# Performance work log

Hardware: AMD Instinct MI355X
Metric: run time of the kernel (lower is better)

## Reference

```python
import jax, jax.numpy as jnp
import numpy as np
from jax import lax

B, C, H, W = 32, 256, 56, 56
OUT_C, K, M = 256, 3, 8
STRIDE = (1, 1)
PADDING = ((1, 1), (1, 1))


def setup_inputs() -> dict:
    key = jax.random.key(0)
    ks = jax.random.split(key, 5)
    x = jax.random.normal(ks[0], (B, C, H, W), dtype=jnp.float32)
    # expert kernels: (M, out_C, in_C/groups, kh, kw), init like torch.randn*0.02
    weight = jax.random.normal(ks[1], (M, OUT_C, C, K, K), dtype=jnp.float32) * 0.02
    bias = jnp.zeros((M, OUT_C), dtype=jnp.float32)
    # gate Linear(in=C, out=M): torch stores weight as (out, in)
    bound = 1.0 / np.sqrt(C)
    gate_w = jax.random.uniform(ks[2], (M, C), minval=-bound, maxval=bound, dtype=jnp.float32)
    gate_b = jax.random.uniform(ks[3], (M,), minval=-bound, maxval=bound, dtype=jnp.float32)
    return {"x": x, "weight": weight, "bias": bias, "gate_w": gate_w, "gate_b": gate_b}


def reference(x, weight, bias, gate_w, gate_b):
    # global average pool -> gating
    gap = jnp.mean(x, axis=(2, 3))                         # (B, C)
    alpha = jax.nn.softmax(gap @ gate_w.T + gate_b, axis=1)  # (B, M)
    # per-sample combined kernels and biases
    kernels = jnp.einsum('bm,moikl->boikl', alpha, weight)  # (B, O, I, k, k)
    biases = alpha @ bias                                   # (B, O)

    def conv_one(xi, wi):
        # xi: (C,H,W), wi: (O,I,k,k)
        out = lax.conv_general_dilated(
            xi[None], wi,
            window_strides=STRIDE, padding=PADDING,
            dimension_numbers=('NCHW', 'OIHW', 'NCHW'))
        return out[0]  # (O, H, W)

    out = jax.vmap(conv_one)(x, kernels)                    # (B, O, H, W)
    return out + biases[:, :, None, None]
```

## Files before the change

kernel.cpp:

```cpp
#include <hip/hip_runtime.h>
#include <hip/hip_bf16.h>

#define B_    32
#define C_    256
#define HW_   3136
#define OC_   256
#define M_    8
#define KPB_  589824

typedef short v8s __attribute__((ext_vector_type(8)));
typedef float f32x4 __attribute__((ext_vector_type(4)));

union bf8pack { v8s v; __hip_bfloat16 h[8]; };

__device__ __forceinline__ void gll16(const short* src, short* dst) {
    __builtin_amdgcn_global_load_lds((const __attribute__((address_space(1))) void*)src,
                                     (__attribute__((address_space(3))) void*)dst, 16, 0, 0);
}

__global__ void zero_gap_kernel(float* __restrict__ gap) {
    gap[blockIdx.x * 256 + threadIdx.x] = 0.f;
}

__global__ __launch_bounds__(256) void xcast_kernel(const float* __restrict__ x,
                                                    short* __restrict__ xg,
                                                    float* __restrict__ gap) {
    __shared__ __hip_bfloat16 tile[64][65];
    int b = blockIdx.z, ct = blockIdx.y, pt = blockIdx.x;
    int p0 = pt*64, c0 = ct*64;
    int tp = threadIdx.x & 63, tc = threadIdx.x >> 6;
    const float* xb = x + ((size_t)b*C_ + c0) * HW_ + p0;
    #pragma unroll
    for (int j = 0; j < 16; ++j) {
        int cl = tc + j*4;
        float v = xb[(size_t)cl*HW_ + tp];
        tile[cl][tp] = __float2bfloat16(v);
        float s = v;
        #pragma unroll
        for (int off = 32; off; off >>= 1) s += __shfl_xor(s, off, 64);
        if (tp == 0) atomicAdd(&gap[b*C_ + c0 + cl], s);
    }
    __syncthreads();
    #pragma unroll
    for (int it = 0; it < 2; ++it) {
        int idx = it*256 + threadIdx.x;
        int px = idx >> 3, ck = idx & 7;
        bf8pack pk;
        #pragma unroll
        for (int j = 0; j < 8; ++j) pk.h[j] = tile[ck*8 + j][px];
        int c = c0 + ck*8;
        size_t dst = (((size_t)b*8 + (c >> 5))*HW_ + p0 + px)*32 + (c & 31);
        *(v8s*)(xg + dst) = pk.v;
    }
}

__global__ void alpha_kernel(const float* __restrict__ gap,
                             const float* __restrict__ gate_w,
                             const float* __restrict__ gate_b,
                             const float* __restrict__ bias,
                             float* __restrict__ alpha,
                             float* __restrict__ biasc) {
    int b = blockIdx.x, lane = threadIdx.x;
    const float inv = 1.0f / HW_;
    float g0 = gap[b*C_ + lane]*inv,       g1 = gap[b*C_ + 64 + lane]*inv;
    float g2 = gap[b*C_ + 128 + lane]*inv, g3 = gap[b*C_ + 192 + lane]*inv;
    float logit[M_];
    #pragma unroll
    for (int m = 0; m < M_; ++m) {
        const float* w = gate_w + m*C_;
        float s = g0*w[lane] + g1*w[64+lane] + g2*w[128+lane] + g3*w[192+lane];
        for (int off = 32; off; off >>= 1) s += __shfl_xor(s, off, 64);
        logit[m] = s + gate_b[m];
    }
    float mx = logit[0];
    #pragma unroll
    for (int m = 1; m < M_; ++m) mx = fmaxf(mx, logit[m]);
    float den = 0.f, e[M_];
    #pragma unroll
    for (int m = 0; m < M_; ++m) { e[m] = __expf(logit[m] - mx); den += e[m]; }
    float am[M_];
    #pragma unroll
    for (int m = 0; m < M_; ++m) am[m] = e[m] / den;
    if (lane < M_) alpha[b*M_ + lane] = am[lane];
    #pragma unroll
    for (int r = 0; r < 4; ++r) {
        int o = r*64 + lane;
        float s = 0.f;
        #pragma unroll
        for (int m = 0; m < M_; ++m) s += am[m] * bias[m*OC_ + o];
        biasc[b*OC_ + o] = s;
    }
}

__global__ __launch_bounds__(256) void combine_kernel(const float* __restrict__ weight,
                                                      const float* __restrict__ alpha,
                                                      short* __restrict__ wl) {
    __shared__ float as[B_*M_];
    as[threadIdx.x] = alpha[threadIdx.x];
    __syncthreads();
    int gc  = blockIdx.x*256 + threadIdx.x;
    int i8  = gc & 3;
    int o   = (gc >> 2) & 255;
    int t2  = gc >> 10;
    int tap = t2 % 9;
    int ib  = t2 / 9;
    int base = o*2304 + (ib*32 + i8*8)*9 + tap;
    float wv[M_][8];
    #pragma unroll
    for (int m = 0; m < M_; ++m)
        #pragma unroll
        for (int j = 0; j < 8; ++j)
            wv[m][j] = weight[(size_t)m*589824 + base + j*9];
    for (int b = 0; b < B_; ++b) {
        bf8pack pk;
        #pragma unroll
        for (int j = 0; j < 8; ++j) {
            float s = 0.f;
            #pragma unroll
            for (int m = 0; m < M_; ++m) s += as[b*M_+m] * wv[m][j];
            pk.h[j] = __float2bfloat16(s);
        }
        *(v8s*)(wl + (size_t)b*KPB_ + (size_t)gc*8) = pk.v;
    }
}

__global__ __launch_bounds__(256, 2) void conv_kernel(const short* __restrict__ xg,
                                                      const short* __restrict__ wl,
                                                      const float* __restrict__ biasc,
                                                      float* __restrict__ out) {
    __shared__ short smem[24576];

    const int wg  = blockIdx.x;
    const int swz = (wg & 7) * 112 + (wg >> 3);
    const int b   = swz / 28;
    const int rm  = swz - b * 28;
    const int ot  = rm / 14;
    const int pt  = rm - ot * 14;

    const int tid = threadIdx.x;
    const int wave = tid >> 6, lane = tid & 63, q = lane >> 4, ln = lane & 15;
    const int o_half = wave >> 1, p_half = wave & 1;
    const int P0 = pt * 224;

    const int DOFF[9] = {-57,-56,-55,-1,0,1,55,56,57};

    unsigned vmask[7];
    #pragma unroll
    for (int c = 0; c < 7; ++c) {
        int p = P0 + p_half*112 + c*16 + ln;
        int h = p/56, w = p%56;
        unsigned m = 0;
        #pragma unroll
        for (int tap = 0; tap < 9; ++tap) {
            int h2 = h + tap/3 - 1, w2 = w + tap%3 - 1;
            if ((unsigned)h2 < 56u && (unsigned)w2 < 56u) m |= (1u << tap);
        }
        vmask[c] = m;
    }

    const short* wbase = wl + (size_t)b*KPB_ + ((ot*128 + o_half*64 + ln)*32 + q*8);
    const short* xbase = xg + (size_t)(b*8)*HW_*32;

    auto stageB = [&](int ib, int buf) {
        const short* src = xbase + ((long)ib*HW_ + P0 - 64)*32 + tid*8;
        short* dst = &smem[buf*12288 + tid*8];
        #pragma unroll
        for (int r = 0; r < 6; ++r) gll16(src + r*2048, dst + r*2048);
    };

    v8s areg[4][4];
    auto loadA = [&](int kidx, v8s (&dst)[4]) {
        const short* src = wbase + (size_t)kidx*8192;
        #pragma unroll
        for (int r = 0; r < 4; ++r) dst[r] = *(const v8s*)(src + r*512);
    };

    f32x4 acc[4][7];
    #pragma unroll
    for (int r = 0; r < 4; ++r)
        #pragma unroll
        for (int c = 0; c < 7; ++c) acc[r][c] = (f32x4){0.f,0.f,0.f,0.f};

    stageB(0, 0);
    loadA(0, areg[0]);
    loadA(1, areg[1]);
    loadA(2, areg[2]);

    const int bcol0 = (64 + p_half*112 + ln)*32 + q*8;
    const v8s vzero = {};

    for (int io = 0; io < 2; ++io) {
        #pragma unroll
        for (int i4 = 0; i4 < 4; ++i4) {
            const int ib = io*4 + i4;
            __syncthreads();
            if (ib < 7) stageB(ib + 1, (i4 + 1) & 1);

            #pragma unroll
            for (int tap = 0; tap < 9; ++tap) {
                const int k = ib*9 + tap;
                if (k + 3 < 72) loadA(k + 3, areg[(i4*9 + tap + 3) & 3]);
                const v8s* A = areg[(i4*9 + tap) & 3];
                const int base = (i4 & 1)*12288 + bcol0 + DOFF[tap]*32;
                #pragma unroll
                for (int c = 0; c < 7; ++c) {
                    v8s v = *(const v8s*)&smem[base + c*512];
                    v8s bf = ((vmask[c] >> tap) & 1) ? v : vzero;
                    #pragma unroll
                    for (int r = 0; r < 4; ++r)
                        acc[r][c] = __builtin_amdgcn_mfma_f32_16x16x32_bf16(A[r], bf, acc[r][c], 0, 0, 0);
                }
            }
        }
    }

    const int o0 = ot*128 + o_half*64 + q*4;
    #pragma unroll
    for (int c = 0; c < 7; ++c) {
        int p = P0 + p_half*112 + c*16 + ln;
        float* op = out + (size_t)b * OC_ * HW_ + p;
        #pragma unroll
        for (int r = 0; r < 4; ++r) {
            #pragma unroll
            for (int reg = 0; reg < 4; ++reg) {
                int o = o0 + r*16 + reg;
                op[(size_t)o * HW_] = acc[r][c][reg] + biasc[b*OC_ + o];
            }
        }
    }
}

extern "C" void kernel_launch(void* const* d_in, const int* in_sizes, int n_in,
                              void* d_out, int out_size, void* d_ws, size_t ws_size,
                              hipStream_t stream) {
    const float* x      = (const float*)d_in[0];
    const float* weight = (const float*)d_in[1];
    const float* bias   = (const float*)d_in[2];
    const float* gate_w = (const float*)d_in[3];
    const float* gate_b = (const float*)d_in[4];
    float* out = (float*)d_out;

    char* ws = (char*)d_ws;
    float* gap   = (float*)(ws);
    float* biasc = (float*)(ws + 32768);
    float* alpha = (float*)(ws + 65536);
    short* xg    = (short*)(ws + 131072);
    short* wl    = (short*)(ws + 51511296);

    zero_gap_kernel<<<32, 256, 0, stream>>>(gap);
    xcast_kernel   <<<dim3(49, 4, 32), 256, 0, stream>>>(x, xg, gap);
    alpha_kernel   <<<32,  64, 0, stream>>>(gap, gate_w, gate_b, bias, alpha, biasc);
    combine_kernel <<<288, 256, 0, stream>>>(weight, alpha, wl);
    conv_kernel    <<<896, 256, 0, stream>>>(xg, wl, biasc, out);
}
```

Measured before the change: 389.7 us.

## Prefetch LDS B fragments one tap ahead and parallelize weight combine over batch

The conv kernel now loads the B operand fragments from LDS one tap ahead into double-buffered registers, so MFMA work overlaps LDS reads. Out-of-bounds taps read from a zeroed LDS slot instead of using a per-element select. The A-operand register prefetch depth drops from three to two to free registers for the extra buffers. Separately, the combine kernel splits the batch loop across 8 y-blocks, giving it 8x more blocks for parallelism at the cost of re-reading the expert weights in each block.

New measurement: 526.8 us. 35.2% more time.

```diff
diff --git a/kernel.cpp b/kernel.cpp
--- a/kernel.cpp
+++ b/kernel.cpp
@@ -111,7 +111,10 @@
         #pragma unroll
         for (int j = 0; j < 8; ++j)
             wv[m][j] = weight[(size_t)m*589824 + base + j*9];
-    for (int b = 0; b < B_; ++b) {
+    int b0 = blockIdx.y * 4;
+    #pragma unroll
+    for (int bi = 0; bi < 4; ++bi) {
+        int b = b0 + bi;
         bf8pack pk;
         #pragma unroll
         for (int j = 0; j < 8; ++j) {
@@ -128,7 +131,8 @@
                                                       const short* __restrict__ wl,
                                                       const float* __restrict__ biasc,
                                                       float* __restrict__ out) {
-    __shared__ short smem[24576];
+    __shared__ short smem[24584];
+    const int ZOFF = 24576;
 
     const int wg  = blockIdx.x;
     const int swz = (wg & 7) * 112 + (wg >> 3);
@@ -168,26 +172,36 @@
         for (int r = 0; r < 6; ++r) gll16(src + r*2048, dst + r*2048);
     };
 
-    v8s areg[4][4];
+    v8s areg[3][4];
     auto loadA = [&](int kidx, v8s (&dst)[4]) {
         const short* src = wbase + (size_t)kidx*8192;
         #pragma unroll
         for (int r = 0; r < 4; ++r) dst[r] = *(const v8s*)(src + r*512);
     };
 
+    const int bcol0 = (64 + p_half*112 + ln)*32 + q*8;
+    auto loadBfrags = [&](int tap, int ibpar, v8s (&dst)[7]) {
+        const int base = ibpar*12288 + bcol0 + DOFF[tap]*32;
+        #pragma unroll
+        for (int c = 0; c < 7; ++c) {
+            int off = ((vmask[c] >> tap) & 1) ? (base + c*512) : ZOFF;
+            dst[c] = *(const v8s*)&smem[off];
+        }
+    };
+
     f32x4 acc[4][7];
     #pragma unroll
     for (int r = 0; r < 4; ++r)
         #pragma unroll
         for (int c = 0; c < 7; ++c) acc[r][c] = (f32x4){0.f,0.f,0.f,0.f};
+
+    if (tid == 0) { *(v8s*)&smem[ZOFF] = (v8s){}; }
 
     stageB(0, 0);
     loadA(0, areg[0]);
     loadA(1, areg[1]);
-    loadA(2, areg[2]);
-
-    const int bcol0 = (64 + p_half*112 + ln)*32 + q*8;
-    const v8s vzero = {};
+
+    v8s brA[7], brB[7];
 
     for (int io = 0; io < 2; ++io) {
         #pragma unroll
@@ -195,20 +209,24 @@
             const int ib = io*4 + i4;
             __syncthreads();
             if (ib < 7) stageB(ib + 1, (i4 + 1) & 1);
+            loadBfrags(0, i4 & 1, brA);
 
             #pragma unroll
             for (int tap = 0; tap < 9; ++tap) {
                 const int k = ib*9 + tap;
-                if (k + 3 < 72) loadA(k + 3, areg[(i4*9 + tap + 3) & 3]);
-                const v8s* A = areg[(i4*9 + tap) & 3];
-                const int base = (i4 & 1)*12288 + bcol0 + DOFF[tap]*32;
+                if (tap < 8) {
+                    if (tap & 1) loadBfrags(tap + 1, i4 & 1, brA);
+                    else         loadBfrags(tap + 1, i4 & 1, brB);
+                }
+                if (k + 2 < 72) loadA(k + 2, areg[(tap + 2) % 3]);
+
+                const v8s* A  = areg[tap % 3];
+                const v8s* Bf = (tap & 1) ? brB : brA;
                 #pragma unroll
                 for (int c = 0; c < 7; ++c) {
-                    v8s v = *(const v8s*)&smem[base + c*512];
-                    v8s bf = ((vmask[c] >> tap) & 1) ? v : vzero;
                     #pragma unroll
                     for (int r = 0; r < 4; ++r)
-                        acc[r][c] = __builtin_amdgcn_mfma_f32_16x16x32_bf16(A[r], bf, acc[r][c], 0, 0, 0);
+                        acc[r][c] = __builtin_amdgcn_mfma_f32_16x16x32_bf16(A[r], Bf[c], acc[r][c], 0, 0, 0);
                 }
             }
         }
@@ -250,6 +268,6 @@
     zero_gap_kernel<<<32, 256, 0, stream>>>(gap);
     xcast_kernel   <<<dim3(49, 4, 32), 256, 0, stream>>>(x, xg, gap);
     alpha_kernel   <<<32,  64, 0, stream>>>(gap, gate_w, gate_b, bias, alpha, biasc);
-    combine_kernel <<<288, 256, 0, stream>>>(weight, alpha, wl);
+    combine_kernel <<<dim3(288, 8), 256, 0, stream>>>(weight, alpha, wl);
     conv_kernel    <<<896, 256, 0, stream>>>(xg, wl, biasc, out);
 }
```
